# Kernel optimization log

Measured on AMD Instinct MI355X. Metric: run time of the kernel, lower is better.

Reference implementation:

```python
import jax, jax.numpy as jnp
import numpy as np
from jax import lax

B, N, W, F = 16, 2000, 32, 5
TH, SH, HEADS = 128, 64, 4
C = SH // HEADS          # per-head out channels = 16
E_BASE = 32000           # base edges per graph


def setup_inputs():
    key = jax.random.key(0)
    ks = jax.random.split(key, 24)
    rn = lambda k, s, sc=0.05: (jax.random.normal(k, s, jnp.float32) * sc)
    inp = {
        'x': jax.random.normal(ks[0], (B, N, W, F), jnp.float32),
        'base_edge_index': jax.random.randint(ks[1], (2, E_BASE), 0, N, jnp.int64),
        # GRU layer 0 (input F -> TH), layer 1 (TH -> TH); PyTorch gate order r,z,n
        'W_ih0': rn(ks[2], (3 * TH, F)), 'W_hh0': rn(ks[3], (3 * TH, TH)),
        'b_ih0': rn(ks[4], (3 * TH,)),   'b_hh0': rn(ks[5], (3 * TH,)),
        'W_ih1': rn(ks[6], (3 * TH, TH)), 'W_hh1': rn(ks[7], (3 * TH, TH)),
        'b_ih1': rn(ks[8], (3 * TH,)),   'b_hh1': rn(ks[9], (3 * TH,)),
        'ln1_g': jnp.ones((TH,), jnp.float32), 'ln1_b': jnp.zeros((TH,), jnp.float32),
        # GATConv: lin (no bias), att_src/att_dst [H,C], output bias [H*C]
        'gat_W': rn(ks[10], (TH, HEADS * C)),
        'att_src': rn(ks[11], (HEADS, C)), 'att_dst': rn(ks[12], (HEADS, C)),
        'gat_b': rn(ks[13], (HEADS * C,)),
        'ln2_g': jnp.ones((SH,), jnp.float32), 'ln2_b': jnp.zeros((SH,), jnp.float32),
        'reg_W1': rn(ks[14], (SH, 32)), 'reg_b1': rn(ks[15], (32,)),
        'reg_W2': rn(ks[16], (32, 1)),  'reg_b2': rn(ks[17], (1,)),
    }
    return inp


def _gru_layer(xs, W_ih, W_hh, b_ih, b_hh):
    # xs: [W, M, Din] time-major; returns (h_T [M,TH], ys [W,M,TH])
    M = xs.shape[1]
    h0 = jnp.zeros((M, W_hh.shape[1]), xs.dtype)

    def step(h, x_t):
        gi = x_t @ W_ih.T + b_ih
        gh = h @ W_hh.T + b_hh
        i_r, i_z, i_n = jnp.split(gi, 3, axis=-1)
        h_r, h_z, h_n = jnp.split(gh, 3, axis=-1)
        r = jax.nn.sigmoid(i_r + h_r)
        z = jax.nn.sigmoid(i_z + h_z)
        n = jnp.tanh(i_n + r * h_n)
        h_new = (1.0 - z) * n + z * h
        return h_new, h_new

    return lax.scan(step, h0, xs)


def _layernorm(x, g, b, eps=1e-5):
    mu = jnp.mean(x, -1, keepdims=True)
    var = jnp.var(x, -1, keepdims=True)
    return (x - mu) * lax.rsqrt(var + eps) * g + b


def _forward(x, base_edge_index, W_ih0, W_hh0, b_ih0, b_hh0, W_ih1, W_hh1,
             b_ih1, b_hh1, ln1_g, ln1_b, gat_W, att_src, att_dst, gat_b,
             ln2_g, ln2_b, reg_W1, reg_b1, reg_W2, reg_b2):
    Bv, Nv, Wv, Fv = x.shape
    M = Bv * Nv
    xs = x.reshape(M, Wv, Fv).transpose(1, 0, 2)  # [W, M, F] time-major
    _, ys0 = _gru_layer(xs, W_ih0, W_hh0, b_ih0, b_hh0)
    h1, _ = _gru_layer(ys0, W_ih1, W_hh1, b_ih1, b_hh1)  # hidden[-1]: [M, TH]
    temb = _layernorm(h1, ln1_g, ln1_b)

    # batched edge index with per-graph node offsets + self loops (PyG default)
    offs = (jnp.arange(Bv, dtype=base_edge_index.dtype) * Nv)
    eb = (base_edge_index[:, None, :] + offs[None, :, None]).reshape(2, -1)
    loops = jnp.arange(M, dtype=base_edge_index.dtype)
    src = jnp.concatenate([eb[0], loops])
    dst = jnp.concatenate([eb[1], loops])

    # GATConv
    xp = (temb @ gat_W).reshape(M, HEADS, C)                 # [M,H,C]
    a_src = jnp.sum(xp * att_src, -1)                        # [M,H]
    a_dst = jnp.sum(xp * att_dst, -1)
    alpha = jax.nn.leaky_relu(a_src[src] + a_dst[dst], 0.2)  # [E,H]
    amax = jax.ops.segment_max(alpha, dst, num_segments=M)
    ex = jnp.exp(alpha - amax[dst])
    den = jax.ops.segment_sum(ex, dst, num_segments=M)
    w = ex / den[dst]                                        # segment softmax
    agg = jax.ops.segment_sum(w[:, :, None] * xp[src], dst, num_segments=M)
    semb = agg.reshape(M, HEADS * C) + gat_b

    semb = jax.nn.leaky_relu(_layernorm(semb, ln2_g, ln2_b), 0.2)
    h = jax.nn.leaky_relu(semb @ reg_W1 + reg_b1, 0.2)
    pred = h @ reg_W2 + reg_b2                               # [M,1]
    return pred.reshape(Bv, Nv)


def reference(x, base_edge_index, W_ih0, W_hh0, b_ih0, b_hh0, W_ih1, W_hh1,
              b_ih1, b_hh1, ln1_g, ln1_b, gat_W, att_src, att_dst, gat_b,
              ln2_g, ln2_b, reg_W1, reg_b1, reg_W2, reg_b2):
    return _forward(x, base_edge_index, W_ih0, W_hh0, b_ih0, b_hh0, W_ih1,
                    W_hh1, b_ih1, b_hh1, ln1_g, ln1_b, gat_W, att_src,
                    att_dst, gat_b, ln2_g, ln2_b, reg_W1, reg_b1, reg_W2,
                    reg_b2)
```

## Files before the change

kernel.cpp:

```cpp
#include <hip/hip_runtime.h>
#include <math.h>

#define B_   16
#define N_   2000
#define W_   32
#define F_   5
#define TH_  128
#define M_   (B_*N_)
#define SH_  64
#define NPB  128

typedef unsigned short u16;
typedef short short8 __attribute__((ext_vector_type(8)));
typedef float f32x4  __attribute__((ext_vector_type(4)));

__device__ __forceinline__ float leaky_(float x) { return x > 0.0f ? x : 0.2f * x; }
__device__ __forceinline__ float sigm_(float x) {
  return __fdividef(1.0f, 1.0f + __expf(-x));
}
__device__ __forceinline__ float tanh_(float x) {
  const float e2 = __expf(2.0f * x);
  return 1.0f - __fdividef(2.0f, e2 + 1.0f);
}

__device__ __forceinline__ u16 f2bf(float f) {
  unsigned u = __float_as_uint(f);
  unsigned r = (u + 0x7FFFu + ((u >> 16) & 1u)) >> 16;
  return (u16)r;
}
__device__ __forceinline__ u16 f2bf_tr(float f) {
  return (u16)(__float_as_uint(f) >> 16);
}
__device__ __forceinline__ float bf2f(u16 h) { return __uint_as_float(((unsigned)h) << 16); }

__device__ __forceinline__ f32x4 mfma3(short8 ah, short8 al, short8 bh, short8 bl, f32x4 c) {
  c = __builtin_amdgcn_mfma_f32_16x16x32_bf16(ah, bh, c, 0, 0, 0);
  c = __builtin_amdgcn_mfma_f32_16x16x32_bf16(al, bh, c, 0, 0, 0);
  c = __builtin_amdgcn_mfma_f32_16x16x32_bf16(ah, bl, c, 0, 0, 0);
  return c;
}

__device__ __forceinline__ void bar_lds() {
  asm volatile("s_waitcnt lgkmcnt(0)" ::: "memory");
  __builtin_amdgcn_s_barrier();
  asm volatile("" ::: "memory");
}

#define S0_ (384*32)
#define S1_ (384*128)
#define XS_ (M_*W_*8)

__global__ void splitA_kernel(const float* __restrict__ Wih0,
                              u16* __restrict__ wih0h, u16* __restrict__ wih0l)
{
  const int i = blockIdx.x * 256 + threadIdx.x;
  if (i >= S0_) return;
  const int row = i >> 5, k = i & 31;
  const float v = (k < F_) ? Wih0[row * F_ + k] : 0.0f;
  const int g = row >> 7, unit = row & 127, wv = unit >> 4, li = unit & 15;
  const int qq = k >> 3, j = k & 7;
  const int p = ((wv * 3 + g) * 64 + qq * 16 + li) * 8 + j;
  const u16 h = f2bf(v);
  wih0h[p] = h;
  wih0l[p] = f2bf(v - bf2f(h));
}

__global__ __launch_bounds__(256)
void splitB_kernel(const float* __restrict__ Whh0, const float* __restrict__ Wih1,
                   const float* __restrict__ Whh1,
                   u16* __restrict__ wpk, u16* __restrict__ wlo)
{
  const int w = blockIdx.x * 4 + (threadIdx.x >> 6);
  const int lane = threadIdx.x & 63;
  const int mat = w / 384;
  const int r = w - mat * 384;
  const float* src = (mat == 0) ? Whh0 : (mat == 1) ? Wih1 : Whh1;
  const int g = r >> 7, unit = r & 127, wv = unit >> 4, li = unit & 15;

#pragma unroll
  for (int e = 0; e < 2; ++e) {
    const int k = lane * 2 + e;
    const float v = src[r * TH_ + k];
    const u16 h = f2bf(v);
    const u16 l = f2bf(v - bf2f(h));
    const int kt = k >> 5, rem = k & 31, qq = rem >> 3, j = rem & 7;
    const int p = (((wv * 3 + mat) * 4 + kt) * 3 + g) * 512 + (qq * 16 + li) * 8 + j;
    wpk[p] = h;
    wlo[p] = l;
  }
}

__global__ __launch_bounds__(256)
void splitX_kernel(const float* __restrict__ x,
                   u16* __restrict__ xh, u16* __restrict__ xl)
{
  const int tid = blockIdx.x * 256 + threadIdx.x;
  if (tid >= M_ * W_) return;
  const int li = tid & 15, nt = (tid >> 4) & 7, t = (tid >> 7) & 31, mb = tid >> 12;
  const int m = mb * NPB + nt * 16 + li;
  const float* px = x + (size_t)m * (W_ * F_) + t * F_;
  short8 vh, vl;
#pragma unroll
  for (int j = 0; j < 8; ++j) {
    const float v = (j < F_) ? px[j] : 0.0f;
    const u16 h = f2bf_tr(v);
    vh[j] = (short)h;
    vl[j] = (short)f2bf(v - bf2f(h));
  }
  *(short8*)(xh + (size_t)tid * 8) = vh;
  *(short8*)(xl + (size_t)tid * 8) = vl;
}

#define POFF(P) ((P) < 4 ? 12288 + (P) * 1536 \
                         : ((P) < 8 ? 6144 + ((P) - 4) * 1536 \
                                    : ((P) - 8) * 1536))

#define WPREF(PN)                                                       \
  { const int o_ = wbase + POFF(PN) + laneo;                            \
    wbh[(PN) & 1][0] = *(const short8*)(wpk + o_);                      \
    wbh[(PN) & 1][1] = *(const short8*)(wpk + o_ + 512);                \
    wbh[(PN) & 1][2] = *(const short8*)(wpk + o_ + 1024);               \
    wbl[(PN) & 1][0] = *(const short8*)(wlo + o_);                      \
    wbl[(PN) & 1][1] = *(const short8*)(wlo + o_ + 512);                \
    wbl[(PN) & 1][2] = *(const short8*)(wlo + o_ + 1024); }

__global__ __launch_bounds__(512, 2)
void gru_mfma_kernel(const u16* __restrict__ xpkh, const u16* __restrict__ xpkl,
                     const u16* __restrict__ wih0h, const u16* __restrict__ wih0l,
                     const u16* __restrict__ wpk, const u16* __restrict__ wlo,
                     const float* __restrict__ bih0, const float* __restrict__ bhh0,
                     const float* __restrict__ bih1, const float* __restrict__ bhh1,
                     const float* __restrict__ ln1g, const float* __restrict__ ln1b,
                     float* __restrict__ temb)
{
  __shared__ u16 h0hi[NPB * TH_], h0lo[NPB * TH_];
  __shared__ u16 h1hi[NPB * TH_], h1lo[NPB * TH_];

  const int tid = threadIdx.x;
  const int lane = tid & 63, wv = tid >> 6, q = lane >> 4, li = lane & 15;
  const int mbase = blockIdx.x * NPB;
  const int unit = wv * 16 + li;
  const int laneo = lane * 8;
  const int wbase = wv * 18432;

  for (int i = tid; i < NPB * TH_ / 2; i += 512) {
    ((unsigned*)h0hi)[i] = 0u; ((unsigned*)h0lo)[i] = 0u;
    ((unsigned*)h1hi)[i] = 0u; ((unsigned*)h1lo)[i] = 0u;
  }

  const float BR0  = bih0[unit] + bhh0[unit];
  const float BZ0  = bih0[TH_ + unit] + bhh0[TH_ + unit];
  const float BNI0 = bih0[2 * TH_ + unit];
  const float BNH0 = bhh0[2 * TH_ + unit];
  const float BR1  = bih1[unit] + bhh1[unit];
  const float BZ1  = bih1[TH_ + unit] + bhh1[TH_ + unit];
  const float BNI1 = bih1[2 * TH_ + unit];
  const float BNH1 = bhh1[2 * TH_ + unit];
  const f32x4 z4 = {0.0f, 0.0f, 0.0f, 0.0f};
  const short8 z8 = {0, 0, 0, 0, 0, 0, 0, 0};

  short8 bih0h_[3], bih0l_[3];
#pragma unroll
  for (int g = 0; g < 3; ++g) {
    const int ro = (wv * 3 + g) * 512 + laneo;
    bih0h_[g] = *(const short8*)(wih0h + ro);
    bih0l_[g] = *(const short8*)(wih0l + ro);
  }

  int nbase[4];
#pragma unroll
  for (int r = 0; r < 4; ++r)
    nbase[r] = (q * 4 + r) * TH_ + ((((unit >> 3) ^ (q * 4 + r))) << 3) + (unit & 7);

  f32x4 aR[8], aZ[8], aNI[8], aNH[8];

  short8 wbh[2][3];
  short8 wbl[2][3];

  {
    const u16* xbh = xpkh + ((size_t)(blockIdx.x * W_ + 0) * 8) * 128 + li * 8;
    const u16* xbl = xpkl + ((size_t)(blockIdx.x * W_ + 0) * 8) * 128 + li * 8;
#pragma unroll
    for (int nt = 0; nt < 8; ++nt) {
      short8 xh8 = z8, xl8 = z8;
      if (q == 0) {
        xh8 = *(const short8*)(xbh + nt * 128);
        xl8 = *(const short8*)(xbl + nt * 128);
      }
#pragma unroll
      for (int g = 0; g < 3; ++g) {
        const f32x4 c = mfma3(xh8, xl8, bih0h_[g], bih0l_[g], z4);
        if (g == 0) aR[nt] = c; else if (g == 1) aZ[nt] = c; else aNI[nt] = c;
      }
      aNH[nt] = z4;
    }
  }
  WPREF(0);

  for (int t = 0; t < W_; ++t) {
    bar_lds();

#pragma unroll
    for (int nt = 0; nt < 8; ++nt)
#pragma unroll
      for (int r = 0; r < 4; ++r) {
        const int idx = nt * 2048 + nbase[r];
        const float hold = bf2f(h0hi[idx]) + bf2f(h0lo[idx]);
        const float rr = sigm_(aR[nt][r] + BR0);
        const float zz = sigm_(aZ[nt][r] + BZ0);
        const float nn = tanh_(aNI[nt][r] + BNI0 + rr * (aNH[nt][r] + BNH0));
        const float hv = (1.0f - zz) * nn + zz * hold;
        const u16 hh = f2bf_tr(hv);
        h0hi[idx] = hh;
        h0lo[idx] = f2bf(hv - bf2f(hh));
      }

#pragma unroll
    for (int kt = 0; kt < 4; ++kt) {
      WPREF(kt + 1);
      const short8 bh0 = wbh[kt & 1][0], bh1 = wbh[kt & 1][1], bh2 = wbh[kt & 1][2];
      const short8 bl0 = wbl[kt & 1][0], bl1 = wbl[kt & 1][1], bl2 = wbl[kt & 1][2];
      const int ko = ((kt * 4 + q) ^ li) * 8;
#pragma unroll
      for (int nt = 0; nt < 8; ++nt) {
        const int ab = (nt * 16 + li) * TH_ + ko;
        const short8 Ah = *(const short8*)(h1hi + ab);
        const short8 Al = *(const short8*)(h1lo + ab);
        aR[nt]  = mfma3(Ah, Al, bh0, bl0, (kt == 0) ? z4 : aR[nt]);
        aZ[nt]  = mfma3(Ah, Al, bh1, bl1, (kt == 0) ? z4 : aZ[nt]);
        aNH[nt] = mfma3(Ah, Al, bh2, bl2, (kt == 0) ? z4 : aNH[nt]);
      }
    }

    bar_lds();

#pragma unroll
    for (int kt = 0; kt < 4; ++kt) {
      const int p = 4 + kt;
      WPREF(p + 1);
      const short8 bh0 = wbh[p & 1][0], bh1 = wbh[p & 1][1], bh2 = wbh[p & 1][2];
      const short8 bl0 = wbl[p & 1][0], bl1 = wbl[p & 1][1], bl2 = wbl[p & 1][2];
      const int ko = ((kt * 4 + q) ^ li) * 8;
#pragma unroll
      for (int nt = 0; nt < 8; ++nt) {
        const int ab = (nt * 16 + li) * TH_ + ko;
        const short8 Ah = *(const short8*)(h0hi + ab);
        const short8 Al = *(const short8*)(h0lo + ab);
        aR[nt]  = mfma3(Ah, Al, bh0, bl0, aR[nt]);
        aZ[nt]  = mfma3(Ah, Al, bh1, bl1, aZ[nt]);
        aNI[nt] = mfma3(Ah, Al, bh2, bl2, (kt == 0) ? z4 : aNI[nt]);
      }
    }

#pragma unroll
    for (int nt = 0; nt < 8; ++nt)
#pragma unroll
      for (int r = 0; r < 4; ++r) {
        const int idx = nt * 2048 + nbase[r];
        const float hold = bf2f(h1hi[idx]) + bf2f(h1lo[idx]);
        const float rr = sigm_(aR[nt][r] + BR1);
        const float zz = sigm_(aZ[nt][r] + BZ1);
        const float nn = tanh_(aNI[nt][r] + BNI1 + rr * (aNH[nt][r] + BNH1));
        const float hv = (1.0f - zz) * nn + zz * hold;
        const u16 hh = f2bf_tr(hv);
        h1hi[idx] = hh;
        h1lo[idx] = f2bf(hv - bf2f(hh));
      }

    if (t < W_ - 1) {
      const u16* xbh = xpkh + ((size_t)(blockIdx.x * W_ + t + 1) * 8) * 128 + li * 8;
      const u16* xbl = xpkl + ((size_t)(blockIdx.x * W_ + t + 1) * 8) * 128 + li * 8;
#pragma unroll
      for (int nt = 0; nt < 8; ++nt) {
        short8 xh8 = z8, xl8 = z8;
        if (q == 0) {
          xh8 = *(const short8*)(xbh + nt * 128);
          xl8 = *(const short8*)(xbl + nt * 128);
        }
#pragma unroll
        for (int g = 0; g < 3; ++g) {
          const f32x4 c = mfma3(xh8, xl8, bih0h_[g], bih0l_[g], z4);
          if (g == 0) aR[nt] = c; else if (g == 1) aZ[nt] = c; else aNI[nt] = c;
        }
      }
#pragma unroll
      for (int kt = 0; kt < 4; ++kt) {
        const int p = 8 + kt;
        WPREF((p + 1) % 12);
        const short8 bh0 = wbh[p & 1][0], bh1 = wbh[p & 1][1], bh2 = wbh[p & 1][2];
        const short8 bl0 = wbl[p & 1][0], bl1 = wbl[p & 1][1], bl2 = wbl[p & 1][2];
        const int ko = ((kt * 4 + q) ^ li) * 8;
#pragma unroll
        for (int nt = 0; nt < 8; ++nt) {
          const int ab = (nt * 16 + li) * TH_ + ko;
          const short8 Ah = *(const short8*)(h0hi + ab);
          const short8 Al = *(const short8*)(h0lo + ab);
          aR[nt]  = mfma3(Ah, Al, bh0, bl0, aR[nt]);
          aZ[nt]  = mfma3(Ah, Al, bh1, bl1, aZ[nt]);
          aNH[nt] = mfma3(Ah, Al, bh2, bl2, (kt == 0) ? z4 : aNH[nt]);
        }
      }
    }
  }
  bar_lds();

  const int n = tid >> 2, qq = tid & 3;
  float vr[32];
  float s = 0.0f;
#pragma unroll
  for (int g8 = 0; g8 < 4; ++g8) {
    const int k0 = qq * 32 + g8 * 8;
    const int g16 = (((k0 >> 3) ^ (n & 15))) * 8;
    const short8 hv = *(const short8*)(h1hi + n * TH_ + g16);
    const short8 lv = *(const short8*)(h1lo + n * TH_ + g16);
#pragma unroll
    for (int j = 0; j < 8; ++j) {
      const float f = bf2f((u16)hv[j]) + bf2f((u16)lv[j]);
      vr[g8 * 8 + j] = f;
      s += f;
    }
  }
  s += __shfl_xor(s, 1, 64); s += __shfl_xor(s, 2, 64);
  const float mu = s * (1.0f / TH_);
  float s2 = 0.0f;
#pragma unroll
  for (int k = 0; k < 32; ++k) { const float d = vr[k] - mu; s2 += d * d; }
  s2 += __shfl_xor(s2, 1, 64); s2 += __shfl_xor(s2, 2, 64);
  const float inv = rsqrtf(s2 * (1.0f / TH_) + 1e-5f);
  float* to = temb + (size_t)(mbase + n) * TH_ + qq * 32;
#pragma unroll
  for (int k = 0; k < 32; ++k)
    to[k] = (vr[k] - mu) * inv * ln1g[qq * 32 + k] + ln1b[qq * 32 + k];
}

__global__ __launch_bounds__(256)
void gat_xp_kernel(const float* __restrict__ temb, const float* __restrict__ gatW,
                   const float* __restrict__ attS, const float* __restrict__ attD,
                   float* __restrict__ xp, float* __restrict__ asrc, float* __restrict__ adst)
{
  __shared__ float ts[64][TH_ + 4];
  __shared__ float4 ws4[TH_][16];
  __shared__ float sa[64], sd[64];

  const int tid = threadIdx.x;
  const int mbase = blockIdx.x * 64;

  for (int i = tid; i < 64 * TH_; i += 256) {
    const int n = i >> 7, k = i & 127;
    ts[n][k] = temb[(size_t)mbase * TH_ + i];
  }
  for (int i = tid; i < TH_ * 16; i += 256)
    ((float4*)ws4)[i] = ((const float4*)gatW)[i];
  if (tid < 64) { sa[tid] = attS[tid]; sd[tid] = attD[tid]; }
  __syncthreads();

  const int nl = tid >> 2;
  const int q  = tid & 3;
  float4 acc[4];
#pragma unroll
  for (int i = 0; i < 4; ++i) acc[i] = make_float4(0.f, 0.f, 0.f, 0.f);

  for (int k = 0; k < TH_; ++k) {
    const float tv = ts[nl][k];
#pragma unroll
    for (int c0 = 0; c0 < 4; ++c0) {
      const float4 wv = ws4[k][q * 4 + c0];
      acc[c0].x += tv * wv.x; acc[c0].y += tv * wv.y;
      acc[c0].z += tv * wv.z; acc[c0].w += tv * wv.w;
    }
  }

  float as = 0.0f, ad = 0.0f;
#pragma unroll
  for (int c0 = 0; c0 < 4; ++c0) {
    const int base = q * 16 + c0 * 4;
    as += acc[c0].x * sa[base + 0] + acc[c0].y * sa[base + 1] +
          acc[c0].z * sa[base + 2] + acc[c0].w * sa[base + 3];
    ad += acc[c0].x * sd[base + 0] + acc[c0].y * sd[base + 1] +
          acc[c0].z * sd[base + 2] + acc[c0].w * sd[base + 3];
  }

  const int m = mbase + nl;
  asrc[m * 4 + q] = as;
  adst[m * 4 + q] = ad;
  float4* xpo = (float4*)&xp[(size_t)m * 64 + q * 16];
#pragma unroll
  for (int c0 = 0; c0 < 4; ++c0) xpo[c0] = acc[c0];
}

__global__ void hist_kernel(const int* __restrict__ ei, const int EB, int* __restrict__ cnt)
{
  const int e = blockIdx.x * 256 + threadIdx.x;
  if (e < EB) atomicAdd(&cnt[ei[EB + e]], 1);
}

__global__ void scan_kernel(const int* __restrict__ cnt, int* __restrict__ offs,
                            int* __restrict__ cursor)
{
  __shared__ int part[256];
  const int tid = threadIdx.x;
  const int c0 = tid * 8;
  int loc[8];
  int s = 0;
#pragma unroll
  for (int j = 0; j < 8; ++j) {
    const int idx = c0 + j;
    const int v = (idx < N_) ? cnt[idx] : 0;
    loc[j] = s; s += v;
  }
  part[tid] = s;
  __syncthreads();
  for (int o = 1; o < 256; o <<= 1) {
    const int v = (tid >= o) ? part[tid - o] : 0;
    __syncthreads();
    part[tid] += v;
    __syncthreads();
  }
  const int base = (tid > 0) ? part[tid - 1] : 0;
#pragma unroll
  for (int j = 0; j < 8; ++j) {
    const int idx = c0 + j;
    if (idx < N_) { offs[idx] = base + loc[j]; cursor[idx] = base + loc[j]; }
  }
  if (tid == 255) offs[N_] = part[255];
}

__global__ void fill_kernel(const int* __restrict__ ei, const int EB,
                            int* __restrict__ cursor, int* __restrict__ ssrc)
{
  const int e = blockIdx.x * 256 + threadIdx.x;
  if (e < EB) {
    const int d = ei[EB + e];
    const int p = atomicAdd(&cursor[d], 1);
    ssrc[p] = ei[e];
  }
}

__global__ __launch_bounds__(256)
void gather_kernel(const int* __restrict__ offs, const int* __restrict__ ssrc,
                   const float* __restrict__ asrc, const float* __restrict__ adst,
                   const float* __restrict__ xp,
                   const float* __restrict__ gatb,
                   const float* __restrict__ ln2g, const float* __restrict__ ln2b,
                   const float* __restrict__ W1, const float* __restrict__ b1,
                   const float* __restrict__ W2, const float* __restrict__ b2,
                   float* __restrict__ out)
{
  __shared__ float sW1[SH_ * 32];
  __shared__ float sb1[32], sW2[32];
  __shared__ float ssemb[4][SH_ + 1];

  const int tid = threadIdx.x;
  for (int i = tid; i < SH_ * 32; i += 256) sW1[i] = W1[i];
  if (tid < 32) { sb1[tid] = b1[tid]; sW2[tid] = W2[tid]; }
  __syncthreads();

  const int lane = tid & 63, grp = tid >> 6;
  const int m = blockIdx.x * 4 + grp;
  const int b = m / N_;
  const int n = m - b * N_;
  const int h = lane >> 4;

  const float adv = adst[m * 4 + h];
  const int o0 = offs[n], o1 = offs[n + 1];
  float accn = 0.0f, accd = 0.0f;
  for (int j = o0; j < o1; ++j) {
    const int s = ssrc[j] + b * N_;
    const float a = asrc[s * 4 + h];
    const float ex = __expf(leaky_(a + adv));
    accn += ex * xp[(size_t)s * 64 + lane];
    accd += ex;
  }
  {
    const float a = asrc[m * 4 + h];
    const float ex = __expf(leaky_(a + adv));
    accn += ex * xp[(size_t)m * 64 + lane];
    accd += ex;
  }

  const float v = accn / accd + gatb[lane];
  float s1 = v;
#pragma unroll
  for (int o = 32; o >= 1; o >>= 1) s1 += __shfl_xor(s1, o, 64);
  const float mu = s1 * (1.0f / 64.0f);
  const float d0 = v - mu;
  float s2 = d0 * d0;
#pragma unroll
  for (int o = 32; o >= 1; o >>= 1) s2 += __shfl_xor(s2, o, 64);
  const float var = s2 * (1.0f / 64.0f);
  float sem = d0 * rsqrtf(var + 1e-5f) * ln2g[lane] + ln2b[lane];
  sem = leaky_(sem);

  ssemb[grp][lane] = sem;
  __syncthreads();

  float contrib = 0.0f;
  if (lane < 32) {
    float acc = sb1[lane];
    for (int c = 0; c < SH_; ++c) acc += ssemb[grp][c] * sW1[c * 32 + lane];
    acc = leaky_(acc);
    contrib = acc * sW2[lane];
  }
#pragma unroll
  for (int o = 32; o >= 1; o >>= 1) contrib += __shfl_xor(contrib, o, 64);
  if (lane == 0) out[m] = contrib + b2[0];
}

extern "C" void kernel_launch(void* const* d_in, const int* in_sizes, int n_in,
                              void* d_out, int out_size, void* d_ws, size_t ws_size,
                              hipStream_t stream)
{
  const float* x    = (const float*)d_in[0];
  const int*   ei   = (const int*)d_in[1];
  const float* Wih0 = (const float*)d_in[2];
  const float* Whh0 = (const float*)d_in[3];
  const float* bih0 = (const float*)d_in[4];
  const float* bhh0 = (const float*)d_in[5];
  const float* Wih1 = (const float*)d_in[6];
  const float* Whh1 = (const float*)d_in[7];
  const float* bih1 = (const float*)d_in[8];
  const float* bhh1 = (const float*)d_in[9];
  const float* ln1g = (const float*)d_in[10];
  const float* ln1b = (const float*)d_in[11];
  const float* gatW = (const float*)d_in[12];
  const float* attS = (const float*)d_in[13];
  const float* attD = (const float*)d_in[14];
  const float* gatb = (const float*)d_in[15];
  const float* ln2g = (const float*)d_in[16];
  const float* ln2b = (const float*)d_in[17];
  const float* W1   = (const float*)d_in[18];
  const float* b1   = (const float*)d_in[19];
  const float* W2   = (const float*)d_in[20];
  const float* b2   = (const float*)d_in[21];
  float* out = (float*)d_out;

  const int EB = in_sizes[1] / 2;

  float* ws = (float*)d_ws;
  float* temb = ws;
  float* xp   = temb + (size_t)M_ * TH_;
  float* asrc = xp + (size_t)M_ * 64;
  float* adst = asrc + (size_t)M_ * 4;
  u16*   wh   = (u16*)(adst + (size_t)M_ * 4);
  u16* wih0h = wh;
  u16* wih0l = wh + S0_;
  u16* wpk   = wh + 2 * S0_;
  u16* wlo   = wpk + 3 * S1_;
  u16* xpkh  = wlo + 3 * S1_;
  u16* xpkl  = xpkh + XS_;
  int* cnt    = (int*)(xpkl + XS_);
  int* offs   = cnt + N_;
  int* cursor = offs + N_ + 1;
  int* ssrc   = cursor + N_;

  splitA_kernel<<<(S0_ + 255) / 256, 256, 0, stream>>>(Wih0, wih0h, wih0l);
  splitB_kernel<<<(3 * 384) / 4, 256, 0, stream>>>(Whh0, Wih1, Whh1, wpk, wlo);
  splitX_kernel<<<(M_ * W_) / 256, 256, 0, stream>>>(x, xpkh, xpkl);

  hipMemsetAsync(cnt, 0, N_ * sizeof(int), stream);
  hist_kernel<<<(EB + 255) / 256, 256, 0, stream>>>(ei, EB, cnt);
  scan_kernel<<<1, 256, 0, stream>>>(cnt, offs, cursor);
  fill_kernel<<<(EB + 255) / 256, 256, 0, stream>>>(ei, EB, cursor, ssrc);

  gru_mfma_kernel<<<M_ / NPB, 512, 0, stream>>>(
      xpkh, xpkl, wih0h, wih0l, wpk, wlo,
      bih0, bhh0, bih1, bhh1, ln1g, ln1b, temb);

  gat_xp_kernel<<<M_ / 64, 256, 0, stream>>>(temb, gatW, attS, attD, xp, asrc, adst);

  gather_kernel<<<M_ / 4, 256, 0, stream>>>(offs, ssrc, asrc, adst, xp,
                                            gatb, ln2g, ln2b, W1, b1, W2, b2, out);
}
```

Before: 1.277 ms.

## Triple-buffer GRU weight prefetch, raise MFMA priority, truncate low bf16 residual

After: 1.445 ms. 13.1% more time.

```diff
diff --git a/kernel.cpp b/kernel.cpp
--- a/kernel.cpp
+++ b/kernel.cpp
@@ -116,13 +116,13 @@
                                     : ((P) - 8) * 1536))
 
 #define WPREF(PN)                                                       \
-  { const int o_ = wbase + POFF(PN) + laneo;                            \
-    wbh[(PN) & 1][0] = *(const short8*)(wpk + o_);                      \
-    wbh[(PN) & 1][1] = *(const short8*)(wpk + o_ + 512);                \
-    wbh[(PN) & 1][2] = *(const short8*)(wpk + o_ + 1024);               \
-    wbl[(PN) & 1][0] = *(const short8*)(wlo + o_);                      \
-    wbl[(PN) & 1][1] = *(const short8*)(wlo + o_ + 512);                \
-    wbl[(PN) & 1][2] = *(const short8*)(wlo + o_ + 1024); }
+  { const int o_ = wbase + POFF((PN) % 12) + laneo;                     \
+    wbh[(PN) % 3][0] = *(const short8*)(wpk + o_);                      \
+    wbh[(PN) % 3][1] = *(const short8*)(wpk + o_ + 512);                \
+    wbh[(PN) % 3][2] = *(const short8*)(wpk + o_ + 1024);               \
+    wbl[(PN) % 3][0] = *(const short8*)(wlo + o_);                      \
+    wbl[(PN) % 3][1] = *(const short8*)(wlo + o_ + 512);                \
+    wbl[(PN) % 3][2] = *(const short8*)(wlo + o_ + 1024); }
 
 __global__ __launch_bounds__(512, 2)
 void gru_mfma_kernel(const u16* __restrict__ xpkh, const u16* __restrict__ xpkl,
@@ -174,8 +174,8 @@
 
   f32x4 aR[8], aZ[8], aNI[8], aNH[8];
 
-  short8 wbh[2][3];
-  short8 wbl[2][3];
+  short8 wbh[3][3];
+  short8 wbl[3][3];
 
   {
     const u16* xbh = xpkh + ((size_t)(blockIdx.x * W_ + 0) * 8) * 128 + li * 8;
@@ -196,6 +196,7 @@
     }
   }
   WPREF(0);
+  WPREF(1);
 
   for (int t = 0; t < W_; ++t) {
     bar_lds();
@@ -212,15 +213,16 @@
         const float hv = (1.0f - zz) * nn + zz * hold;
         const u16 hh = f2bf_tr(hv);
         h0hi[idx] = hh;
-        h0lo[idx] = f2bf(hv - bf2f(hh));
+        h0lo[idx] = f2bf_tr(hv - bf2f(hh));
       }
 
 #pragma unroll
     for (int kt = 0; kt < 4; ++kt) {
-      WPREF(kt + 1);
-      const short8 bh0 = wbh[kt & 1][0], bh1 = wbh[kt & 1][1], bh2 = wbh[kt & 1][2];
-      const short8 bl0 = wbl[kt & 1][0], bl1 = wbl[kt & 1][1], bl2 = wbl[kt & 1][2];
+      WPREF(kt + 2);
+      const short8 bh0 = wbh[kt % 3][0], bh1 = wbh[kt % 3][1], bh2 = wbh[kt % 3][2];
+      const short8 bl0 = wbl[kt % 3][0], bl1 = wbl[kt % 3][1], bl2 = wbl[kt % 3][2];
       const int ko = ((kt * 4 + q) ^ li) * 8;
+      __builtin_amdgcn_s_setprio(1);
 #pragma unroll
       for (int nt = 0; nt < 8; ++nt) {
         const int ab = (nt * 16 + li) * TH_ + ko;
@@ -230,6 +232,7 @@
         aZ[nt]  = mfma3(Ah, Al, bh1, bl1, (kt == 0) ? z4 : aZ[nt]);
         aNH[nt] = mfma3(Ah, Al, bh2, bl2, (kt == 0) ? z4 : aNH[nt]);
       }
+      __builtin_amdgcn_s_setprio(0);
     }
 
     bar_lds();
@@ -237,10 +240,11 @@
 #pragma unroll
     for (int kt = 0; kt < 4; ++kt) {
       const int p = 4 + kt;
-      WPREF(p + 1);
-      const short8 bh0 = wbh[p & 1][0], bh1 = wbh[p & 1][1], bh2 = wbh[p & 1][2];
-      const short8 bl0 = wbl[p & 1][0], bl1 = wbl[p & 1][1], bl2 = wbl[p & 1][2];
+      WPREF(p + 2);
+      const short8 bh0 = wbh[p % 3][0], bh1 = wbh[p % 3][1], bh2 = wbh[p % 3][2];
+      const short8 bl0 = wbl[p % 3][0], bl1 = wbl[p % 3][1], bl2 = wbl[p % 3][2];
       const int ko = ((kt * 4 + q) ^ li) * 8;
+      __builtin_amdgcn_s_setprio(1);
 #pragma unroll
       for (int nt = 0; nt < 8; ++nt) {
         const int ab = (nt * 16 + li) * TH_ + ko;
@@ -250,6 +254,7 @@
         aZ[nt]  = mfma3(Ah, Al, bh1, bl1, aZ[nt]);
         aNI[nt] = mfma3(Ah, Al, bh2, bl2, (kt == 0) ? z4 : aNI[nt]);
       }
+      __builtin_amdgcn_s_setprio(0);
     }
 
 #pragma unroll
@@ -264,7 +269,7 @@
         const float hv = (1.0f - zz) * nn + zz * hold;
         const u16 hh = f2bf_tr(hv);
         h1hi[idx] = hh;
-        h1lo[idx] = f2bf(hv - bf2f(hh));
+        h1lo[idx] = f2bf_tr(hv - bf2f(hh));
       }
 
     if (t < W_ - 1) {
@@ -286,10 +291,11 @@
 #pragma unroll
       for (int kt = 0; kt < 4; ++kt) {
         const int p = 8 + kt;
-        WPREF((p + 1) % 12);
-        const short8 bh0 = wbh[p & 1][0], bh1 = wbh[p & 1][1], bh2 = wbh[p & 1][2];
-        const short8 bl0 = wbl[p & 1][0], bl1 = wbl[p & 1][1], bl2 = wbl[p & 1][2];
+        WPREF(p + 2);
+        const short8 bh0 = wbh[p % 3][0], bh1 = wbh[p % 3][1], bh2 = wbh[p % 3][2];
+        const short8 bl0 = wbl[p % 3][0], bl1 = wbl[p % 3][1], bl2 = wbl[p % 3][2];
         const int ko = ((kt * 4 + q) ^ li) * 8;
+        __builtin_amdgcn_s_setprio(1);
 #pragma unroll
         for (int nt = 0; nt < 8; ++nt) {
           const int ab = (nt * 16 + li) * TH_ + ko;
@@ -299,6 +305,7 @@
           aZ[nt]  = mfma3(Ah, Al, bh1, bl1, aZ[nt]);
           aNH[nt] = mfma3(Ah, Al, bh2, bl2, (kt == 0) ? z4 : aNH[nt]);
         }
+        __builtin_amdgcn_s_setprio(0);
       }
     }
   }
```
